# Kernel optimization log

Measured on AMD Instinct MI355X. Metric: run time of the kernel, lower is better.

Reference implementation:

```python
import jax, jax.numpy as jnp
import numpy as np

B, LSEQ, LQ = 16, 1024, 256
N_CTX, BIN = 8, 256
D, H, DEPTH = 1024, 16, 6
DFF = 4096
NEG = -1e9


def _ln(x, s, b, eps=1e-5):
    m = jnp.mean(x, axis=-1, keepdims=True)
    v = jnp.var(x, axis=-1, keepdims=True)
    return (x - m) * jax.lax.rsqrt(v + eps) * s + b


def setup_inputs() -> dict:
    key = jax.random.key(0)
    ks = jax.random.split(key, 16)
    s = 0.02
    return {
        "latents": jax.random.normal(ks[0], (B, LSEQ, D), jnp.float32),
        "in_time_idx": jax.random.randint(ks[1], (B, LSEQ), 0, BIN),
        "in_space_idx": jax.random.randint(ks[2], (B, LSEQ), 0, 32),
        "in_mask": jnp.ones((B, N_CTX + LSEQ), dtype=bool),
        "query_idx": jax.random.randint(ks[3], (B, LQ), 0, 2),
        "query_time_idx": jnp.sort(jax.random.randint(ks[4], (B, LQ), 0, BIN), axis=1),
        "query_space_idx": jax.random.randint(ks[5], (B, LQ), 0, 32),
        "query_mask": jnp.ones((B, LQ), dtype=bool),
        "ctx_emb": jax.random.normal(ks[6], (B, N_CTX, D), jnp.float32),
        "query_emb_w": s * jax.random.normal(ks[7], (2, D), jnp.float32),
        "time_emb_w": s * jax.random.normal(ks[8], (BIN, D), jnp.float32),
        "qkv_w": s * jax.random.normal(ks[9], (DEPTH, 3 * D, D), jnp.float32),
        "qkv_b": jnp.zeros((DEPTH, 3 * D), jnp.float32),
        "out_w": s * jax.random.normal(ks[10], (DEPTH, D, D), jnp.float32),
        "out_b": jnp.zeros((DEPTH, D), jnp.float32),
        "ln1_s": jnp.ones((DEPTH, D), jnp.float32),
        "ln1_b": jnp.zeros((DEPTH, D), jnp.float32),
        "ln2_s": jnp.ones((DEPTH, D), jnp.float32),
        "ln2_b": jnp.zeros((DEPTH, D), jnp.float32),
        "w1": s * jax.random.normal(ks[11], (DEPTH, DFF, D), jnp.float32),
        "b1": jnp.zeros((DEPTH, DFF), jnp.float32),
        "w2": s * jax.random.normal(ks[12], (DEPTH, D, DFF), jnp.float32),
        "b2": jnp.zeros((DEPTH, D), jnp.float32),
    }


def reference(latents, in_time_idx, in_space_idx, in_mask, query_idx,
              query_time_idx, query_space_idx, query_mask, ctx_emb,
              query_emb_w, time_emb_w, qkv_w, qkv_b, out_w, out_b,
              ln1_s, ln1_b, ln2_s, ln2_b, w1, b1, w2, b2):
    # ---- _pool: scatter-reduce mean of latents into (B, BIN, D) ----
    seq_mask = in_mask[:, N_CTX:]                               # (B, LSEQ)
    idx = jnp.where(seq_mask, in_time_idx, BIN)                 # masked -> trash bin
    oneh = jax.nn.one_hot(idx, BIN + 1, dtype=latents.dtype)    # (B, LSEQ, BIN+1)
    sums = jnp.einsum('bls,bld->bsd', oneh, latents)            # (B, BIN+1, D)
    cnts = jnp.sum(oneh, axis=1)                                # (B, BIN+1)
    pooled = (sums / jnp.maximum(cnts, 1.0)[:, :, None])[:, :BIN]

    pooled_time = jnp.broadcast_to(jnp.arange(BIN), (B, BIN))
    dec_time_idx = jnp.concatenate([pooled_time, query_time_idx], axis=1)  # (B, BIN+LQ)

    x = jnp.concatenate([pooled, query_emb_w[query_idx]], axis=1)
    x = x + time_emb_w[dec_time_idx]
    x = jnp.concatenate([jax.lax.stop_gradient(ctx_emb), x], axis=1)  # (B, L, D)
    L = N_CTX + BIN + LQ

    # ---- per-sample causal + context attention mask (True = blocked) ----
    blocked = jnp.zeros((B, L, L), dtype=bool)
    blocked = blocked.at[:, :N_CTX, N_CTX:].set(True)
    blocked = blocked.at[:, N_CTX:, N_CTX:].set(
        dec_time_idx[:, :, None] < dec_time_idx[:, None, :])
    pad = jnp.concatenate([jnp.zeros((B, N_CTX + BIN), bool), ~query_mask], axis=1)
    blocked = blocked | pad[:, None, :]
    bias = jnp.where(blocked, NEG, 0.0).astype(x.dtype)[:, None]  # (B,1,L,L)

    dh = D // H
    scale = 1.0 / np.sqrt(dh).astype(np.float32)

    def layer(h, p):
        qw, qb, ow, ob, l1s, l1b, l2s, l2b, fw1, fb1, fw2, fb2 = p
        # pre-norm self-attention
        y = _ln(h, l1s, l1b)
        qkv = y @ qw.T + qb
        q, k, v = jnp.split(qkv, 3, axis=-1)
        q = q.reshape(B, L, H, dh)
        k = k.reshape(B, L, H, dh)
        v = v.reshape(B, L, H, dh)
        scores = jnp.einsum('bihd,bjhd->bhij', q, k) * scale + bias
        a = jax.nn.softmax(scores, axis=-1)
        o = jnp.einsum('bhij,bjhd->bihd', a, v).reshape(B, L, D)
        h = h + o @ ow.T + ob
        # pre-norm FFN (exact GELU, as torch default)
        y = _ln(h, l2s, l2b)
        h = h + jax.nn.gelu(y @ fw1.T + fb1, approximate=False) @ fw2.T + fb2
        return h, None

    x, _ = jax.lax.scan(
        layer, x,
        (qkv_w, qkv_b, out_w, out_b, ln1_s, ln1_b, ln2_s, ln2_b, w1, b1, w2, b2))
    return x[:, N_CTX:]  # (B, BIN+LQ, D)
```

## Files before the change

### kernel.cpp

```cpp
#include <hip/hip_runtime.h>

#define B_    16
#define NCTX  8
#define BIN_  256
#define LQ_   256
#define L_    520
#define LSEQ  1024
#define D_    1024
#define H_    16
#define DH    64
#define DFF_  4096
#define DEPTH 6
#define MROWS (B_ * L_)
#define GY    65

using bf16x8 = __attribute__((ext_vector_type(8))) __bf16;
using bf16x4 = __attribute__((ext_vector_type(4))) __bf16;
using f32x4  = __attribute__((ext_vector_type(4))) float;

#define DEV __device__ __forceinline__

DEV int swz(int r, int c) { return (r << 6) + (((c ^ r) & 7) << 3); }

#define GLDS16(g, l)                                                         \
  __builtin_amdgcn_global_load_lds(                                          \
      (__attribute__((address_space(1))) void*)(g),                          \
      (__attribute__((address_space(3))) void*)(l), 16, 0, 0)


__global__ void te_k(const int* __restrict__ qtime, int* __restrict__ Te,
                     int* __restrict__ TeMinK, int* __restrict__ TeMaxQ) {
  int b = blockIdx.x, pos = threadIdx.x;
  __shared__ int smin[9], smax[9];
  if (pos < 9) { smin[pos] = 0x7fffffff; smax[pos] = (int)0x80000000; }
  __syncthreads();
  int v;
  if (pos < NCTX) v = (int)0x80000000;
  else if (pos < NCTX + BIN_) v = pos - NCTX;
  else if (pos < L_) v = qtime[b * LQ_ + (pos - NCTX - BIN_)];
  else v = 0x7fffffff;
  Te[b * 576 + pos] = v;
  int vq = (pos < L_) ? v : (int)0x80000000;
  atomicMin(&smin[pos >> 6], v);
  atomicMax(&smax[pos >> 6], vq);
  __syncthreads();
  if (pos < 9) { TeMinK[b * 9 + pos] = smin[pos]; TeMaxQ[b * 9 + pos] = smax[pos]; }
}

__global__ void pool_k(const float* __restrict__ latents,
                       const int* __restrict__ tIdx,
                       const float* __restrict__ temb, float* __restrict__ h) {
  int s = blockIdx.x, b = blockIdx.y, tid = threadIdx.x;
  __shared__ int sIdx[LSEQ];
#pragma unroll
  for (int j = 0; j < 4; ++j) sIdx[tid + 256 * j] = tIdx[b * LSEQ + tid + 256 * j];
  __syncthreads();
  float a0 = 0.f, a1 = 0.f, a2 = 0.f, a3 = 0.f;
  int cnt = 0;
  const float4* L = (const float4*)(latents + (size_t)b * LSEQ * D_);
  for (int l = 0; l < LSEQ; ++l) {
    if (sIdx[l] == s) {
      float4 v = L[(size_t)l * 256 + tid];
      a0 += v.x; a1 += v.y; a2 += v.z; a3 += v.w; ++cnt;
    }
  }
  float inv = 1.f / (float)(cnt > 0 ? cnt : 1);
  float4 te = ((const float4*)(temb + (size_t)s * D_))[tid];
  float4 o;
  o.x = a0 * inv + te.x; o.y = a1 * inv + te.y;
  o.z = a2 * inv + te.z; o.w = a3 * inv + te.w;
  ((float4*)(h + ((size_t)b * L_ + NCTX + s) * D_))[tid] = o;
}

__global__ void qrows_k(const float* __restrict__ ctx,
                        const float* __restrict__ qemb,
                        const float* __restrict__ temb,
                        const int* __restrict__ qidx,
                        const int* __restrict__ qtime, float* __restrict__ h) {
  int r = blockIdx.x, b = blockIdx.y, tid = threadIdx.x;
  if (r < NCTX) {
    float4 v = ((const float4*)(ctx + ((size_t)b * NCTX + r) * D_))[tid];
    ((float4*)(h + ((size_t)b * L_ + r) * D_))[tid] = v;
  } else {
    int q = r - NCTX;
    int qi = qidx[b * LQ_ + q];
    int qt = qtime[b * LQ_ + q];
    float4 e = ((const float4*)(qemb + (size_t)qi * D_))[tid];
    float4 t = ((const float4*)(temb + (size_t)qt * D_))[tid];
    float4 o; o.x = e.x + t.x; o.y = e.y + t.y; o.z = e.z + t.z; o.w = e.w + t.w;
    ((float4*)(h + ((size_t)b * L_ + NCTX + BIN_ + q) * D_))[tid] = o;
  }
}

__global__ void cvt4_k(const float* __restrict__ s0, const float* __restrict__ s1,
                       const float* __restrict__ s2, const float* __restrict__ s3,
                       __bf16* __restrict__ dst) {
  int i = blockIdx.x * 256 + threadIdx.x;
  const float* s; int off;
  if (i < 786432)       { s = s0; off = i; }
  else if (i < 1048576) { s = s1; off = i - 786432; }
  else if (i < 2097152) { s = s2; off = i - 1048576; }
  else                  { s = s3; off = i - 2097152; }
  float4 v = ((const float4*)s)[off];
  bf16x4 o;
  o[0] = (__bf16)v.x; o[1] = (__bf16)v.y; o[2] = (__bf16)v.z; o[3] = (__bf16)v.w;
  ((bf16x4*)dst)[i] = o;
}

__global__ __launch_bounds__(256) void ln_k(const float* __restrict__ h,
                                            const float* __restrict__ s,
                                            const float* __restrict__ bb,
                                            __bf16* __restrict__ y) {
  int row = blockIdx.x, tid = threadIdx.x;
  int lane = tid & 63, wave = tid >> 6;
  float4 v = ((const float4*)(h + (size_t)row * D_))[tid];
  float sum = v.x + v.y + v.z + v.w;
  float sq  = v.x * v.x + v.y * v.y + v.z * v.z + v.w * v.w;
#pragma unroll
  for (int m = 32; m; m >>= 1) { sum += __shfl_xor(sum, m); sq += __shfl_xor(sq, m); }
  __shared__ float red[8];
  if (lane == 0) { red[wave] = sum; red[4 + wave] = sq; }
  __syncthreads();
  sum = red[0] + red[1] + red[2] + red[3];
  sq  = red[4] + red[5] + red[6] + red[7];
  float mean = sum * (1.f / D_);
  float var  = sq * (1.f / D_) - mean * mean;
  float rstd = rsqrtf(var + 1e-5f);
  float4 sv = ((const float4*)s)[tid];
  float4 bv = ((const float4*)bb)[tid];
  bf16x4 o;
  o[0] = (__bf16)((v.x - mean) * rstd * sv.x + bv.x);
  o[1] = (__bf16)((v.y - mean) * rstd * sv.y + bv.y);
  o[2] = (__bf16)((v.z - mean) * rstd * sv.z + bv.z);
  o[3] = (__bf16)((v.w - mean) * rstd * sv.w + bv.w);
  *(bf16x4*)(y + (size_t)row * D_ + tid * 4) = o;
}

template <int EPI>
__global__ __launch_bounds__(256) void gemm_k(const __bf16* __restrict__ A,
                                              const __bf16* __restrict__ Bw,
                                              const float* __restrict__ bias,
                                              __bf16* __restrict__ outB,
                                              float* __restrict__ outF,
                                              int N, int K, int gx) {
  __shared__ __bf16 sA[128 * 64];
  __shared__ __bf16 sB[128 * 64];
  const int tid = threadIdx.x;
  const int lane = tid & 63, wave = tid >> 6;
  const int lr = lane & 15, lq = lane >> 4;
  const int wr = wave >> 1, wc = wave & 1;

  const int nwg = gridDim.x;
  int hid = blockIdx.x;
  int lid = (hid & 7) * (nwg >> 3) + (hid >> 3);
  int per_band = gx << 3;
  int band = lid / per_band;
  int rem = lid - band * per_band;
  int rows = min(8, GY - (band << 3));
  int by = (band << 3) + rem % rows;
  int bx = rem / rows;
  const size_t bm = (size_t)by * 128;
  const size_t bn = (size_t)bx * 128;

  f32x4 acc[4][4] = {};

  int stage_r[4], stage_src[4];
#pragma unroll
  for (int j = 0; j < 4; ++j) {
    int q = (wave * 4 + j) * 64 + lane;
    int r = q >> 3, c = q & 7;
    stage_r[j] = r;
    stage_src[j] = ((c ^ r) & 7) << 3;
  }
  const __bf16* Ab = A + bm * (size_t)K;
  const __bf16* Bb = Bw + bn * (size_t)K;
  const int nk = K >> 6;
  for (int kt = 0; kt < nk; ++kt) {
    const __bf16* Ak = Ab + kt * 64;
    const __bf16* Bk = Bb + kt * 64;
#pragma unroll
    for (int j = 0; j < 4; ++j) {
      int r = stage_r[j];
      GLDS16(Ak + (size_t)r * K + stage_src[j], sA + (wave * 4 + j) * 512);
      GLDS16(Bk + (size_t)r * K + stage_src[j], sB + (wave * 4 + j) * 512);
    }
    __syncthreads();
#pragma unroll
    for (int kk = 0; kk < 2; ++kk) {
      bf16x8 af[4], bfm[4];
#pragma unroll
      for (int im = 0; im < 4; ++im)
        af[im] = *(const bf16x8*)(sA + swz(wr * 64 + im * 16 + lr, kk * 4 + lq));
#pragma unroll
      for (int in = 0; in < 4; ++in)
        bfm[in] = *(const bf16x8*)(sB + swz(wc * 64 + in * 16 + lr, kk * 4 + lq));
#pragma unroll
      for (int im = 0; im < 4; ++im)
#pragma unroll
        for (int in = 0; in < 4; ++in)
          acc[im][in] = __builtin_amdgcn_mfma_f32_16x16x32_bf16(af[im], bfm[in], acc[im][in], 0, 0, 0);
    }
    __syncthreads();
  }
  const int r0 = (int)bm + wr * 64 + lq * 4;
  const int c0 = (int)bn + wc * 64 + lr;
#pragma unroll
  for (int in = 0; in < 4; ++in) {
    int cg = c0 + in * 16;
    float bl = bias[cg];
#pragma unroll
    for (int im = 0; im < 4; ++im) {
      f32x4 v = acc[im][in];
#pragma unroll
      for (int i = 0; i < 4; ++i) {
        int rg = r0 + im * 16 + i;
        float val = v[i] + bl;
        if (EPI == 0) {
          outB[(size_t)rg * N + cg] = (__bf16)val;
        } else if (EPI == 1) {
          outF[(size_t)rg * N + cg] += val;
        } else {
          float g = 0.5f * val * (1.0f + erff(val * 0.70710678118f));
          outB[(size_t)rg * N + cg] = (__bf16)g;
        }
      }
    }
  }
}

__global__ __launch_bounds__(256) void attn_k(const __bf16* __restrict__ qkv,
                                              const int* __restrict__ Te,
                                              const int* __restrict__ TeMinK,
                                              const int* __restrict__ TeMaxQ,
                                              __bf16* __restrict__ o) {
  const int qt = blockIdx.x, hh = blockIdx.y, b = blockIdx.z;
  const int tid = threadIdx.x;
  const int lane = tid & 63, wave = tid >> 6;
  const int lr = lane & 15, lq = lane >> 4;
  __shared__ __bf16 sQ[64 * 64], sK[64 * 64], sV[64 * 64];
  __shared__ __bf16 sP[4][16 * 64];
  __shared__ int sTq[64], sTk[64];

  if (tid < 64) sTq[tid] = Te[b * 576 + qt * 64 + tid];
  const int maxQ = TeMaxQ[b * 9 + qt];

  const __bf16* base = qkv + (size_t)b * L_ * (3 * D_) + hh * DH;
#pragma unroll
  for (int j = 0; j < 2; ++j) {
    int q = tid + j * 256;
    int r = q >> 3, c = q & 7;
    int rg = qt * 64 + r;
    bf16x8 v = {};
    if (rg < L_) v = *(const bf16x8*)(base + (size_t)rg * (3 * D_) + c * 8);
    *(bf16x8*)(sQ + swz(r, c)) = v;
  }

  float m_run[4], l_run[4];
#pragma unroll
  for (int i = 0; i < 4; ++i) { m_run[i] = -1e30f; l_run[i] = 0.f; }
  f32x4 oacc[4] = {};
  const float scale = 0.125f;

  for (int kt = 0; kt < 9; ++kt) {
    if (TeMinK[b * 9 + kt] > maxQ) continue;
    __syncthreads();
    if (tid < 64) sTk[tid] = Te[b * 576 + kt * 64 + tid];
#pragma unroll
    for (int j = 0; j < 2; ++j) {
      int q = tid + j * 256;
      int r = q >> 3, c = q & 7;
      int rg = kt * 64 + r;
      bf16x8 kv = {}, vv = {};
      if (rg < L_) {
        kv = *(const bf16x8*)(base + D_ + (size_t)rg * (3 * D_) + c * 8);
        vv = *(const bf16x8*)(base + 2 * D_ + (size_t)rg * (3 * D_) + c * 8);
      }
      *(bf16x8*)(sK + swz(r, c)) = kv;
      *(bf16x8*)(sV + r * 64 + c * 8) = vv;
    }
    __syncthreads();

    f32x4 sacc[4] = {};
#pragma unroll
    for (int kk = 0; kk < 2; ++kk) {
      bf16x8 aq = *(const bf16x8*)(sQ + swz(wave * 16 + lr, kk * 4 + lq));
#pragma unroll
      for (int cn = 0; cn < 4; ++cn) {
        bf16x8 bk = *(const bf16x8*)(sK + swz(cn * 16 + lr, kk * 4 + lq));
        sacc[cn] = __builtin_amdgcn_mfma_f32_16x16x32_bf16(aq, bk, sacc[cn], 0, 0, 0);
      }
    }
    float sval[4][4], mt[4];
#pragma unroll
    for (int i = 0; i < 4; ++i) mt[i] = -1e30f;
#pragma unroll
    for (int cn = 0; cn < 4; ++cn) {
      int tk = sTk[cn * 16 + lr];
#pragma unroll
      for (int i = 0; i < 4; ++i) {
        int tq = sTq[wave * 16 + lq * 4 + i];
        float sv = sacc[cn][i] * scale + ((tq < tk) ? -1e9f : 0.f);
        sval[cn][i] = sv;
        mt[i] = fmaxf(mt[i], sv);
      }
    }
#pragma unroll
    for (int i = 0; i < 4; ++i) {
#pragma unroll
      for (int m = 1; m < 16; m <<= 1) mt[i] = fmaxf(mt[i], __shfl_xor(mt[i], m));
    }
    float fsc[4], lt[4];
    __bf16* sPw = sP[wave];
#pragma unroll
    for (int i = 0; i < 4; ++i) {
      float mnew = fmaxf(m_run[i], mt[i]);
      fsc[i] = __expf(m_run[i] - mnew);
      m_run[i] = mnew;
      lt[i] = 0.f;
    }
#pragma unroll
    for (int cn = 0; cn < 4; ++cn) {
#pragma unroll
      for (int i = 0; i < 4; ++i) {
        float p = __expf(sval[cn][i] - m_run[i]);
        lt[i] += p;
        int rp = lq * 4 + i;
        int kvx = cn * 16 + lr;
        sPw[(rp << 6) + ((((kvx >> 3) ^ rp) & 7) << 3) + (kvx & 7)] = (__bf16)p;
      }
    }
#pragma unroll
    for (int i = 0; i < 4; ++i) {
#pragma unroll
      for (int m = 1; m < 16; m <<= 1) lt[i] += __shfl_xor(lt[i], m);
      l_run[i] = l_run[i] * fsc[i] + lt[i];
    }
#pragma unroll
    for (int dn = 0; dn < 4; ++dn)
#pragma unroll
      for (int i = 0; i < 4; ++i) oacc[dn][i] *= fsc[i];

#pragma unroll
    for (int kk = 0; kk < 2; ++kk) {
      bf16x8 ap = *(const bf16x8*)(sPw + swz(lr, kk * 4 + lq));
#pragma unroll
      for (int dn = 0; dn < 4; ++dn) {
        bf16x8 bv;
#pragma unroll
        for (int i2 = 0; i2 < 8; ++i2)
          bv[i2] = sV[(kk * 32 + lq * 8 + i2) * 64 + dn * 16 + lr];
        oacc[dn] = __builtin_amdgcn_mfma_f32_16x16x32_bf16(ap, bv, oacc[dn], 0, 0, 0);
      }
    }
  }
#pragma unroll
  for (int dn = 0; dn < 4; ++dn) {
#pragma unroll
    for (int i = 0; i < 4; ++i) {
      int rg = qt * 64 + wave * 16 + lq * 4 + i;
      if (rg < L_) {
        float val = oacc[dn][i] / l_run[i];
        o[((size_t)b * L_ + rg) * D_ + hh * DH + dn * 16 + lr] = (__bf16)val;
      }
    }
  }
}

__global__ void out_k(const float* __restrict__ h, float* __restrict__ out) {
  int idx = blockIdx.x * 256 + threadIdx.x;
  int c4 = idx & 255;
  int r = (idx >> 8) & 511;
  int b = idx >> 17;
  ((float4*)out)[idx] = ((const float4*)h)[((size_t)b * L_ + NCTX + r) * 256 + c4];
}

extern "C" void kernel_launch(void* const* d_in, const int* in_sizes, int n_in,
                              void* d_out, int out_size, void* d_ws, size_t ws_size,
                              hipStream_t stream) {
  const float* latents      = (const float*)d_in[0];
  const int*   in_time_idx  = (const int*)d_in[1];
  const int*   query_idx    = (const int*)d_in[4];
  const int*   query_time   = (const int*)d_in[5];
  const float* ctx_emb      = (const float*)d_in[8];
  const float* query_emb_w  = (const float*)d_in[9];
  const float* time_emb_w   = (const float*)d_in[10];
  const float* qkv_w        = (const float*)d_in[11];
  const float* qkv_b        = (const float*)d_in[12];
  const float* out_w        = (const float*)d_in[13];
  const float* out_b        = (const float*)d_in[14];
  const float* ln1_s        = (const float*)d_in[15];
  const float* ln1_b        = (const float*)d_in[16];
  const float* ln2_s        = (const float*)d_in[17];
  const float* ln2_b        = (const float*)d_in[18];
  const float* w1           = (const float*)d_in[19];
  const float* b1           = (const float*)d_in[20];
  const float* w2           = (const float*)d_in[21];
  const float* b2           = (const float*)d_in[22];

  size_t off = 0;
  auto alloc = [&](size_t n) { char* p = (char*)d_ws + off; off += (n + 255) & ~(size_t)255; return (void*)p; };
  float*  h    = (float*)alloc((size_t)MROWS * D_ * 4);
  __bf16* y    = (__bf16*)alloc((size_t)MROWS * D_ * 2);
  __bf16* qkvb = (__bf16*)alloc((size_t)MROWS * 3 * D_ * 2);
  __bf16* mid  = (__bf16*)alloc((size_t)MROWS * DFF_ * 2);
  __bf16* wsl  = (__bf16*)alloc((size_t)12582912 * 2);
  int*    Te   = (int*)alloc((size_t)B_ * 576 * 4);
  int*    TeMn = (int*)alloc((size_t)B_ * 9 * 4);
  int*    TeMx = (int*)alloc((size_t)B_ * 9 * 4);
  (void)ws_size; (void)in_sizes; (void)n_in; (void)out_size;
  __bf16* wq  = wsl;
  __bf16* wo  = wsl + 3145728;
  __bf16* w1b = wsl + 4194304;
  __bf16* w2b = wsl + 8388608;

  te_k<<<B_, 576, 0, stream>>>(query_time, Te, TeMn, TeMx);
  pool_k<<<dim3(BIN_, B_), 256, 0, stream>>>(latents, in_time_idx, time_emb_w, h);
  qrows_k<<<dim3(NCTX + LQ_, B_), 256, 0, stream>>>(ctx_emb, query_emb_w, time_emb_w,
                                                    query_idx, query_time, h);
  for (int l = 0; l < DEPTH; ++l) {
    cvt4_k<<<12288, 256, 0, stream>>>(qkv_w + (size_t)l * 3145728, out_w + (size_t)l * 1048576,
                                      w1 + (size_t)l * 4194304, w2 + (size_t)l * 4194304, wsl);

    ln_k<<<MROWS, 256, 0, stream>>>(h, ln1_s + l * D_, ln1_b + l * D_, y);
    gemm_k<0><<<24 * GY, 256, 0, stream>>>(
        y, wq, qkv_b + (size_t)l * 3 * D_, qkvb, nullptr, 3 * D_, D_, 24);
    attn_k<<<dim3(9, H_, B_), 256, 0, stream>>>(qkvb, Te, TeMn, TeMx, y);
    gemm_k<1><<<8 * GY, 256, 0, stream>>>(
        y, wo, out_b + (size_t)l * D_, nullptr, h, D_, D_, 8);
    ln_k<<<MROWS, 256, 0, stream>>>(h, ln2_s + l * D_, ln2_b + l * D_, y);
    gemm_k<2><<<32 * GY, 256, 0, stream>>>(
        y, w1b, b1 + (size_t)l * DFF_, mid, nullptr, DFF_, D_, 32);
    gemm_k<1><<<8 * GY, 256, 0, stream>>>(
        mid, w2b, b2 + (size_t)l * D_, nullptr, h, D_, DFF_, 8);
  }
  out_k<<<(B_ * 512 * 256) / 256, 256, 0, stream>>>(h, (float*)d_out);
}
```

Measured before the change: 3.014 ms.

## Double-buffer GEMM LDS tiles, rewrite pooling as scatter-add, raise attention MFMA priority

The GEMM main loop now uses two LDS buffers, so the global-to-LDS load of the next K tile is issued before the current tile is computed. This overlaps memory latency with MFMA work, at the cost of twice the shared memory per block, which may lower occupancy. The pooling kernel no longer has each bin block scan all 1024 rows. It scatters rows into LDS accumulators with atomics and takes the per-bin counts from a histogram built in te_k. The attention kernel also raises wave priority around its MFMA sections.

```diff
diff --git a/kernel.cpp b/kernel.cpp
--- a/kernel.cpp
+++ b/kernel.cpp
@@ -28,11 +28,13 @@
       (__attribute__((address_space(3))) void*)(l), 16, 0, 0)
 
 
-__global__ void te_k(const int* __restrict__ qtime, int* __restrict__ Te,
-                     int* __restrict__ TeMinK, int* __restrict__ TeMaxQ) {
+__global__ void te_k(const int* __restrict__ qtime, const int* __restrict__ tIdx,
+                     int* __restrict__ Te, int* __restrict__ TeMinK,
+                     int* __restrict__ TeMaxQ, int* __restrict__ cnts) {
   int b = blockIdx.x, pos = threadIdx.x;
-  __shared__ int smin[9], smax[9];
+  __shared__ int smin[9], smax[9], hc[256];
   if (pos < 9) { smin[pos] = 0x7fffffff; smax[pos] = (int)0x80000000; }
+  if (pos < 256) hc[pos] = 0;
   __syncthreads();
   int v;
   if (pos < NCTX) v = (int)0x80000000;
@@ -43,33 +45,36 @@
   int vq = (pos < L_) ? v : (int)0x80000000;
   atomicMin(&smin[pos >> 6], v);
   atomicMax(&smax[pos >> 6], vq);
+  for (int i = pos; i < LSEQ; i += 576) atomicAdd(&hc[tIdx[b * LSEQ + i]], 1);
   __syncthreads();
   if (pos < 9) { TeMinK[b * 9 + pos] = smin[pos]; TeMaxQ[b * 9 + pos] = smax[pos]; }
-}
-
-__global__ void pool_k(const float* __restrict__ latents,
-                       const int* __restrict__ tIdx,
-                       const float* __restrict__ temb, float* __restrict__ h) {
-  int s = blockIdx.x, b = blockIdx.y, tid = threadIdx.x;
+  if (pos < 256) cnts[b * 256 + pos] = hc[pos];
+}
+
+__global__ __launch_bounds__(256) void pool_k(const float* __restrict__ latents,
+                                              const int* __restrict__ tIdx,
+                                              const int* __restrict__ cnts,
+                                              const float* __restrict__ temb,
+                                              float* __restrict__ h) {
+  const int cg = blockIdx.x, b = blockIdx.y, tid = threadIdx.x;
+  __shared__ float acc[256][33];
   __shared__ int sIdx[LSEQ];
+  float* af = &acc[0][0];
+  for (int i = tid; i < 256 * 33; i += 256) af[i] = 0.f;
 #pragma unroll
   for (int j = 0; j < 4; ++j) sIdx[tid + 256 * j] = tIdx[b * LSEQ + tid + 256 * j];
   __syncthreads();
-  float a0 = 0.f, a1 = 0.f, a2 = 0.f, a3 = 0.f;
-  int cnt = 0;
-  const float4* L = (const float4*)(latents + (size_t)b * LSEQ * D_);
-  for (int l = 0; l < LSEQ; ++l) {
-    if (sIdx[l] == s) {
-      float4 v = L[(size_t)l * 256 + tid];
-      a0 += v.x; a1 += v.y; a2 += v.z; a3 += v.w; ++cnt;
-    }
-  }
-  float inv = 1.f / (float)(cnt > 0 ? cnt : 1);
-  float4 te = ((const float4*)(temb + (size_t)s * D_))[tid];
-  float4 o;
-  o.x = a0 * inv + te.x; o.y = a1 * inv + te.y;
-  o.z = a2 * inv + te.z; o.w = a3 * inv + te.w;
-  ((float4*)(h + ((size_t)b * L_ + NCTX + s) * D_))[tid] = o;
+  const int col = tid & 31, rp = tid >> 5;
+  const float* Lb = latents + (size_t)b * LSEQ * D_ + cg * 32 + col;
+  for (int r = rp; r < LSEQ; r += 8)
+    atomicAdd(&acc[sIdx[r]][col], Lb[(size_t)r * D_]);
+  __syncthreads();
+  for (int s = rp; s < 256; s += 8) {
+    int c = cnts[b * 256 + s];
+    float inv = 1.f / (float)(c > 0 ? c : 1);
+    h[((size_t)b * L_ + NCTX + s) * D_ + cg * 32 + col] =
+        acc[s][col] * inv + temb[(size_t)s * D_ + cg * 32 + col];
+  }
 }
 
 __global__ void qrows_k(const float* __restrict__ ctx,
@@ -136,6 +141,32 @@
   *(bf16x4*)(y + (size_t)row * D_ + tid * 4) = o;
 }
 
+#define GSTAGE(kt, P)                                                         \
+  do {                                                                        \
+    const __bf16* _Ak = Ab + (size_t)(kt) * 64;                               \
+    const __bf16* _Bk = Bb + (size_t)(kt) * 64;                               \
+    _Pragma("unroll") for (int _j = 0; _j < 4; ++_j) {                        \
+      int _r = stage_r[_j];                                                   \
+      GLDS16(_Ak + (size_t)_r * K + stage_src[_j], sA[P] + (wave * 4 + _j) * 512); \
+      GLDS16(_Bk + (size_t)_r * K + stage_src[_j], sB[P] + (wave * 4 + _j) * 512); \
+    }                                                                         \
+  } while (0)
+
+#define GCOMPUTE(P)                                                           \
+  do {                                                                        \
+    _Pragma("unroll") for (int _kk = 0; _kk < 2; ++_kk) {                     \
+      bf16x8 _af[4], _bf[4];                                                  \
+      _Pragma("unroll") for (int _im = 0; _im < 4; ++_im)                     \
+        _af[_im] = *(const bf16x8*)(sA[P] + swz(wr * 64 + _im * 16 + lr, _kk * 4 + lq)); \
+      _Pragma("unroll") for (int _in = 0; _in < 4; ++_in)                     \
+        _bf[_in] = *(const bf16x8*)(sB[P] + swz(wc * 64 + _in * 16 + lr, _kk * 4 + lq)); \
+      _Pragma("unroll") for (int _im = 0; _im < 4; ++_im)                     \
+        _Pragma("unroll") for (int _in = 0; _in < 4; ++_in)                   \
+          acc[_im][_in] = __builtin_amdgcn_mfma_f32_16x16x32_bf16(            \
+              _af[_im], _bf[_in], acc[_im][_in], 0, 0, 0);                    \
+    }                                                                         \
+  } while (0)
+
 template <int EPI>
 __global__ __launch_bounds__(256) void gemm_k(const __bf16* __restrict__ A,
                                               const __bf16* __restrict__ Bw,
@@ -143,8 +174,8 @@
                                               __bf16* __restrict__ outB,
                                               float* __restrict__ outF,
                                               int N, int K, int gx) {
-  __shared__ __bf16 sA[128 * 64];
-  __shared__ __bf16 sB[128 * 64];
+  __shared__ __bf16 sA[2][128 * 64];
+  __shared__ __bf16 sB[2][128 * 64];
   const int tid = threadIdx.x;
   const int lane = tid & 63, wave = tid >> 6;
   const int lr = lane & 15, lq = lane >> 4;
@@ -175,33 +206,18 @@
   const __bf16* Ab = A + bm * (size_t)K;
   const __bf16* Bb = Bw + bn * (size_t)K;
   const int nk = K >> 6;
-  for (int kt = 0; kt < nk; ++kt) {
-    const __bf16* Ak = Ab + kt * 64;
-    const __bf16* Bk = Bb + kt * 64;
-#pragma unroll
-    for (int j = 0; j < 4; ++j) {
-      int r = stage_r[j];
-      GLDS16(Ak + (size_t)r * K + stage_src[j], sA + (wave * 4 + j) * 512);
-      GLDS16(Bk + (size_t)r * K + stage_src[j], sB + (wave * 4 + j) * 512);
-    }
+
+  GSTAGE(0, 0);
+  __syncthreads();
+  for (int it = 0; it < nk; it += 2) {
+    if (it + 1 < nk) GSTAGE(it + 1, 1);
+    GCOMPUTE(0);
     __syncthreads();
-#pragma unroll
-    for (int kk = 0; kk < 2; ++kk) {
-      bf16x8 af[4], bfm[4];
-#pragma unroll
-      for (int im = 0; im < 4; ++im)
-        af[im] = *(const bf16x8*)(sA + swz(wr * 64 + im * 16 + lr, kk * 4 + lq));
-#pragma unroll
-      for (int in = 0; in < 4; ++in)
-        bfm[in] = *(const bf16x8*)(sB + swz(wc * 64 + in * 16 + lr, kk * 4 + lq));
-#pragma unroll
-      for (int im = 0; im < 4; ++im)
-#pragma unroll
-        for (int in = 0; in < 4; ++in)
-          acc[im][in] = __builtin_amdgcn_mfma_f32_16x16x32_bf16(af[im], bfm[in], acc[im][in], 0, 0, 0);
-    }
+    if (it + 2 < nk) GSTAGE(it + 2, 0);
+    GCOMPUTE(1);
     __syncthreads();
   }
+
   const int r0 = (int)bm + wr * 64 + lq * 4;
   const int c0 = (int)bn + wc * 64 + lr;
 #pragma unroll
@@ -281,6 +297,7 @@
     __syncthreads();
 
     f32x4 sacc[4] = {};
+    __builtin_amdgcn_s_setprio(1);
 #pragma unroll
     for (int kk = 0; kk < 2; ++kk) {
       bf16x8 aq = *(const bf16x8*)(sQ + swz(wave * 16 + lr, kk * 4 + lq));
@@ -290,6 +307,7 @@
         sacc[cn] = __builtin_amdgcn_mfma_f32_16x16x32_bf16(aq, bk, sacc[cn], 0, 0, 0);
       }
     }
+    __builtin_amdgcn_s_setprio(0);
     float sval[4][4], mt[4];
 #pragma unroll
     for (int i = 0; i < 4; ++i) mt[i] = -1e30f;
@@ -340,6 +358,7 @@
 #pragma unroll
       for (int i = 0; i < 4; ++i) oacc[dn][i] *= fsc[i];
 
+    __builtin_amdgcn_s_setprio(1);
 #pragma unroll
     for (int kk = 0; kk < 2; ++kk) {
       bf16x8 ap = *(const bf16x8*)(sPw + swz(lr, kk * 4 + lq));
@@ -352,6 +371,7 @@
         oacc[dn] = __builtin_amdgcn_mfma_f32_16x16x32_bf16(ap, bv, oacc[dn], 0, 0, 0);
       }
     }
+    __builtin_amdgcn_s_setprio(0);
   }
 #pragma unroll
   for (int dn = 0; dn < 4; ++dn) {
@@ -407,14 +427,15 @@
   int*    Te   = (int*)alloc((size_t)B_ * 576 * 4);
   int*    TeMn = (int*)alloc((size_t)B_ * 9 * 4);
   int*    TeMx = (int*)alloc((size_t)B_ * 9 * 4);
+  int*    Cnt  = (int*)alloc((size_t)B_ * 256 * 4);
   (void)ws_size; (void)in_sizes; (void)n_in; (void)out_size;
   __bf16* wq  = wsl;
   __bf16* wo  = wsl + 3145728;
   __bf16* w1b = wsl + 4194304;
   __bf16* w2b = wsl + 8388608;
 
-  te_k<<<B_, 576, 0, stream>>>(query_time, Te, TeMn, TeMx);
-  pool_k<<<dim3(BIN_, B_), 256, 0, stream>>>(latents, in_time_idx, time_emb_w, h);
+  te_k<<<B_, 576, 0, stream>>>(query_time, in_time_idx, Te, TeMn, TeMx, Cnt);
+  pool_k<<<dim3(32, B_), 256, 0, stream>>>(latents, in_time_idx, Cnt, time_emb_w, h);
   qrows_k<<<dim3(NCTX + LQ_, B_), 256, 0, stream>>>(ctx_emb, query_emb_w, time_emb_w,
                                                     query_idx, query_time, h);
   for (int l = 0; l < DEPTH; ++l) {
```

Measured after the change: 3.285 ms. 1.09x slower.

## Rewrite pooling as LDS scatter-add and enlarge attention query tiles to 128 rows

Applied to the files above, without the earlier changes.

The pooling kernel used to scan all sequence positions once per bin, which read the latents with a branch per position. It now streams the latents once per 32-column slice, accumulating into a shared-memory histogram with atomics, and the per-bin counts are precomputed in te_k. The attention kernel now processes 128 query rows per block with 512 threads, so each K/V tile load is reused by twice as many queries, and it adds s_setprio around the MFMA sections. The risks are LDS atomic contention in pooling and coarser tile skipping, since the causal skip test now uses the max over two query tiles.

```diff
diff --git a/kernel.cpp b/kernel.cpp
--- a/kernel.cpp
+++ b/kernel.cpp
@@ -28,11 +28,13 @@
       (__attribute__((address_space(3))) void*)(l), 16, 0, 0)
 
 
-__global__ void te_k(const int* __restrict__ qtime, int* __restrict__ Te,
-                     int* __restrict__ TeMinK, int* __restrict__ TeMaxQ) {
+__global__ void te_k(const int* __restrict__ qtime, const int* __restrict__ tIdx,
+                     int* __restrict__ Te, int* __restrict__ TeMinK,
+                     int* __restrict__ TeMaxQ, int* __restrict__ cnts) {
   int b = blockIdx.x, pos = threadIdx.x;
-  __shared__ int smin[9], smax[9];
+  __shared__ int smin[9], smax[9], hc[256];
   if (pos < 9) { smin[pos] = 0x7fffffff; smax[pos] = (int)0x80000000; }
+  if (pos < 256) hc[pos] = 0;
   __syncthreads();
   int v;
   if (pos < NCTX) v = (int)0x80000000;
@@ -43,33 +45,36 @@
   int vq = (pos < L_) ? v : (int)0x80000000;
   atomicMin(&smin[pos >> 6], v);
   atomicMax(&smax[pos >> 6], vq);
+  for (int i = pos; i < LSEQ; i += 576) atomicAdd(&hc[tIdx[b * LSEQ + i]], 1);
   __syncthreads();
   if (pos < 9) { TeMinK[b * 9 + pos] = smin[pos]; TeMaxQ[b * 9 + pos] = smax[pos]; }
-}
-
-__global__ void pool_k(const float* __restrict__ latents,
-                       const int* __restrict__ tIdx,
-                       const float* __restrict__ temb, float* __restrict__ h) {
-  int s = blockIdx.x, b = blockIdx.y, tid = threadIdx.x;
+  if (pos < 256) cnts[b * 256 + pos] = hc[pos];
+}
+
+__global__ __launch_bounds__(256) void pool_k(const float* __restrict__ latents,
+                                              const int* __restrict__ tIdx,
+                                              const int* __restrict__ cnts,
+                                              const float* __restrict__ temb,
+                                              float* __restrict__ h) {
+  const int cg = blockIdx.x, b = blockIdx.y, tid = threadIdx.x;
+  __shared__ float acc[256][33];
   __shared__ int sIdx[LSEQ];
+  float* af = &acc[0][0];
+  for (int i = tid; i < 256 * 33; i += 256) af[i] = 0.f;
 #pragma unroll
   for (int j = 0; j < 4; ++j) sIdx[tid + 256 * j] = tIdx[b * LSEQ + tid + 256 * j];
   __syncthreads();
-  float a0 = 0.f, a1 = 0.f, a2 = 0.f, a3 = 0.f;
-  int cnt = 0;
-  const float4* L = (const float4*)(latents + (size_t)b * LSEQ * D_);
-  for (int l = 0; l < LSEQ; ++l) {
-    if (sIdx[l] == s) {
-      float4 v = L[(size_t)l * 256 + tid];
-      a0 += v.x; a1 += v.y; a2 += v.z; a3 += v.w; ++cnt;
-    }
-  }
-  float inv = 1.f / (float)(cnt > 0 ? cnt : 1);
-  float4 te = ((const float4*)(temb + (size_t)s * D_))[tid];
-  float4 o;
-  o.x = a0 * inv + te.x; o.y = a1 * inv + te.y;
-  o.z = a2 * inv + te.z; o.w = a3 * inv + te.w;
-  ((float4*)(h + ((size_t)b * L_ + NCTX + s) * D_))[tid] = o;
+  const int col = tid & 31, rp = tid >> 5;
+  const float* Lb = latents + (size_t)b * LSEQ * D_ + cg * 32 + col;
+  for (int r = rp; r < LSEQ; r += 8)
+    atomicAdd(&acc[sIdx[r]][col], Lb[(size_t)r * D_]);
+  __syncthreads();
+  for (int s = rp; s < 256; s += 8) {
+    int c = cnts[b * 256 + s];
+    float inv = 1.f / (float)(c > 0 ? c : 1);
+    h[((size_t)b * L_ + NCTX + s) * D_ + cg * 32 + col] =
+        acc[s][col] * inv + temb[(size_t)s * D_ + cg * 32 + col];
+  }
 }
 
 __global__ void qrows_k(const float* __restrict__ ctx,
@@ -228,7 +233,7 @@
   }
 }
 
-__global__ __launch_bounds__(256) void attn_k(const __bf16* __restrict__ qkv,
+__global__ __launch_bounds__(512) void attn_k(const __bf16* __restrict__ qkv,
                                               const int* __restrict__ Te,
                                               const int* __restrict__ TeMinK,
                                               const int* __restrict__ TeMaxQ,
@@ -237,19 +242,23 @@
   const int tid = threadIdx.x;
   const int lane = tid & 63, wave = tid >> 6;
   const int lr = lane & 15, lq = lane >> 4;
-  __shared__ __bf16 sQ[64 * 64], sK[64 * 64], sV[64 * 64];
-  __shared__ __bf16 sP[4][16 * 64];
-  __shared__ int sTq[64], sTk[64];
-
-  if (tid < 64) sTq[tid] = Te[b * 576 + qt * 64 + tid];
-  const int maxQ = TeMaxQ[b * 9 + qt];
+  __shared__ __bf16 sQ[128 * 64], sK[64 * 64], sV[64 * 64];
+  __shared__ __bf16 sP[8][16 * 64];
+  __shared__ int sTq[128], sTk[64];
+
+  if (tid < 128) {
+    int rg = qt * 128 + tid;
+    sTq[tid] = (rg < 576) ? Te[b * 576 + rg] : 0x7fffffff;
+  }
+  int maxQ = TeMaxQ[b * 9 + qt * 2];
+  if (qt * 2 + 1 < 9) maxQ = max(maxQ, TeMaxQ[b * 9 + qt * 2 + 1]);
 
   const __bf16* base = qkv + (size_t)b * L_ * (3 * D_) + hh * DH;
 #pragma unroll
   for (int j = 0; j < 2; ++j) {
-    int q = tid + j * 256;
+    int q = tid + j * 512;
     int r = q >> 3, c = q & 7;
-    int rg = qt * 64 + r;
+    int rg = qt * 128 + r;
     bf16x8 v = {};
     if (rg < L_) v = *(const bf16x8*)(base + (size_t)rg * (3 * D_) + c * 8);
     *(bf16x8*)(sQ + swz(r, c)) = v;
@@ -265,10 +274,8 @@
     if (TeMinK[b * 9 + kt] > maxQ) continue;
     __syncthreads();
     if (tid < 64) sTk[tid] = Te[b * 576 + kt * 64 + tid];
-#pragma unroll
-    for (int j = 0; j < 2; ++j) {
-      int q = tid + j * 256;
-      int r = q >> 3, c = q & 7;
+    {
+      int r = tid >> 3, c = tid & 7;
       int rg = kt * 64 + r;
       bf16x8 kv = {}, vv = {};
       if (rg < L_) {
@@ -281,6 +288,7 @@
     __syncthreads();
 
     f32x4 sacc[4] = {};
+    __builtin_amdgcn_s_setprio(1);
 #pragma unroll
     for (int kk = 0; kk < 2; ++kk) {
       bf16x8 aq = *(const bf16x8*)(sQ + swz(wave * 16 + lr, kk * 4 + lq));
@@ -290,6 +298,7 @@
         sacc[cn] = __builtin_amdgcn_mfma_f32_16x16x32_bf16(aq, bk, sacc[cn], 0, 0, 0);
       }
     }
+    __builtin_amdgcn_s_setprio(0);
     float sval[4][4], mt[4];
 #pragma unroll
     for (int i = 0; i < 4; ++i) mt[i] = -1e30f;
@@ -340,6 +349,7 @@
 #pragma unroll
       for (int i = 0; i < 4; ++i) oacc[dn][i] *= fsc[i];
 
+    __builtin_amdgcn_s_setprio(1);
 #pragma unroll
     for (int kk = 0; kk < 2; ++kk) {
       bf16x8 ap = *(const bf16x8*)(sPw + swz(lr, kk * 4 + lq));
@@ -352,12 +362,13 @@
         oacc[dn] = __builtin_amdgcn_mfma_f32_16x16x32_bf16(ap, bv, oacc[dn], 0, 0, 0);
       }
     }
+    __builtin_amdgcn_s_setprio(0);
   }
 #pragma unroll
   for (int dn = 0; dn < 4; ++dn) {
 #pragma unroll
     for (int i = 0; i < 4; ++i) {
-      int rg = qt * 64 + wave * 16 + lq * 4 + i;
+      int rg = qt * 128 + wave * 16 + lq * 4 + i;
       if (rg < L_) {
         float val = oacc[dn][i] / l_run[i];
         o[((size_t)b * L_ + rg) * D_ + hh * DH + dn * 16 + lr] = (__bf16)val;
@@ -407,14 +418,15 @@
   int*    Te   = (int*)alloc((size_t)B_ * 576 * 4);
   int*    TeMn = (int*)alloc((size_t)B_ * 9 * 4);
   int*    TeMx = (int*)alloc((size_t)B_ * 9 * 4);
+  int*    Cnt  = (int*)alloc((size_t)B_ * 256 * 4);
   (void)ws_size; (void)in_sizes; (void)n_in; (void)out_size;
   __bf16* wq  = wsl;
   __bf16* wo  = wsl + 3145728;
   __bf16* w1b = wsl + 4194304;
   __bf16* w2b = wsl + 8388608;
 
-  te_k<<<B_, 576, 0, stream>>>(query_time, Te, TeMn, TeMx);
-  pool_k<<<dim3(BIN_, B_), 256, 0, stream>>>(latents, in_time_idx, time_emb_w, h);
+  te_k<<<B_, 576, 0, stream>>>(query_time, in_time_idx, Te, TeMn, TeMx, Cnt);
+  pool_k<<<dim3(32, B_), 256, 0, stream>>>(latents, in_time_idx, Cnt, time_emb_w, h);
   qrows_k<<<dim3(NCTX + LQ_, B_), 256, 0, stream>>>(ctx_emb, query_emb_w, time_emb_w,
                                                     query_idx, query_time, h);
   for (int l = 0; l < DEPTH; ++l) {
@@ -424,7 +436,7 @@
     ln_k<<<MROWS, 256, 0, stream>>>(h, ln1_s + l * D_, ln1_b + l * D_, y);
     gemm_k<0><<<24 * GY, 256, 0, stream>>>(
         y, wq, qkv_b + (size_t)l * 3 * D_, qkvb, nullptr, 3 * D_, D_, 24);
-    attn_k<<<dim3(9, H_, B_), 256, 0, stream>>>(qkvb, Te, TeMn, TeMx, y);
+    attn_k<<<dim3(5, H_, B_), 512, 0, stream>>>(qkvb, Te, TeMn, TeMx, y);
     gemm_k<1><<<8 * GY, 256, 0, stream>>>(
         y, wo, out_b + (size_t)l * D_, nullptr, h, D_, D_, 8);
     ln_k<<<MROWS, 256, 0, stream>>>(h, ln2_s + l * D_, ln2_b + l * D_, y);
```

Measured after the change: 3.055 ms. No clear change (+1.4%).
